# Performance work log

Measured on AMD Instinct MI355X. Metric: run time of the kernel, lower is better.

Reference implementation:

```python
import jax, jax.numpy as jnp
import numpy as np

N = 30000          # nodes
E = 480000         # edges (before self-loops)
G = 64             # graphs in batch
EMB = 64
IN = 6 + 2 * EMB   # 134
H1, C1 = 4, 128    # gat1 heads / out channels
H2, C2 = 1, 256    # gat2
LRELU_SLOPE = 0.2


def _layernorm(x, g, b, eps=1e-5):
    m = x.mean(-1, keepdims=True)
    v = ((x - m) ** 2).mean(-1, keepdims=True)
    return (x - m) / jnp.sqrt(v + eps) * g + b


def _gatv2(x, src, dst, Wl, bl, Wr, br, att, bias, H, C, n, concat):
    # GATv2 (PyG semantics, share_weights=False, eval mode -> no dropout)
    xl = (x @ Wl + bl).reshape(n, H, C)   # source transform
    xr = (x @ Wr + br).reshape(n, H, C)   # target transform
    # e_ij = att . leaky_relu(xl_j + xr_i), edges j->i : [E_tot, H]
    e = jnp.sum(jax.nn.leaky_relu(xl[src] + xr[dst], LRELU_SLOPE) * att, axis=-1)
    # scatter-softmax over incoming edges of each target node
    emax = jax.lax.stop_gradient(jax.ops.segment_max(e, dst, num_segments=n))
    ex = jnp.exp(e - emax[dst])
    den = jax.ops.segment_sum(ex, dst, num_segments=n)
    alpha = ex / (den[dst] + 1e-16)                       # [E_tot, H]
    out = jax.ops.segment_sum(alpha[:, :, None] * xl[src], dst, num_segments=n)
    if concat:
        return out.reshape(n, H * C) + bias
    return out.mean(axis=1) + bias


def setup_inputs() -> dict:
    key = jax.random.key(0)
    ks = jax.random.split(key, 24)
    s = 0.05
    inp = {
        "x_cont": jax.random.normal(ks[0], (N, 6), jnp.float32),
        "x_class": jax.random.randint(ks[1], (N,), 0, 12, jnp.int32),
        "x_pitch": jax.random.randint(ks[2], (N,), 0, 129, jnp.int32),
        "edge_index": jax.random.randint(ks[3], (2, E), 0, N, jnp.int32),
        "batch": jnp.sort(jax.random.randint(ks[4], (N,), 0, G, jnp.int32)),
        "class_tab": jax.random.normal(ks[5], (12, EMB), jnp.float32) * s,
        "pitch_tab": jax.random.normal(ks[6], (129, EMB), jnp.float32) * s,
        "Wl1": jax.random.normal(ks[7], (IN, H1 * C1), jnp.float32) * s,
        "bl1": jnp.zeros((H1 * C1,), jnp.float32),
        "Wr1": jax.random.normal(ks[8], (IN, H1 * C1), jnp.float32) * s,
        "br1": jnp.zeros((H1 * C1,), jnp.float32),
        "att1": jax.random.normal(ks[9], (H1, C1), jnp.float32) * s,
        "bias1": jnp.zeros((H1 * C1,), jnp.float32),
        "ln1_g": jnp.ones((H1 * C1,), jnp.float32),
        "ln1_b": jnp.zeros((H1 * C1,), jnp.float32),
        "Wl2": jax.random.normal(ks[10], (H1 * C1, H2 * C2), jnp.float32) * s,
        "bl2": jnp.zeros((H2 * C2,), jnp.float32),
        "Wr2": jax.random.normal(ks[11], (H1 * C1, H2 * C2), jnp.float32) * s,
        "br2": jnp.zeros((H2 * C2,), jnp.float32),
        "att2": jax.random.normal(ks[12], (H2, C2), jnp.float32) * s,
        "bias2": jnp.zeros((C2,), jnp.float32),
        "ln2_g": jnp.ones((C2,), jnp.float32),
        "ln2_b": jnp.zeros((C2,), jnp.float32),
        "Wp1": jax.random.normal(ks[13], (C2, 512), jnp.float32) * s,
        "bp1": jnp.zeros((512,), jnp.float32),
        "lnp_g": jnp.ones((512,), jnp.float32),
        "lnp_b": jnp.zeros((512,), jnp.float32),
        "Wp2": jax.random.normal(ks[14], (512, 512), jnp.float32) * s,
        "bp2": jnp.zeros((512,), jnp.float32),
    }
    return inp


def reference(x_cont, x_class, x_pitch, edge_index, batch,
              class_tab, pitch_tab,
              Wl1, bl1, Wr1, br1, att1, bias1, ln1_g, ln1_b,
              Wl2, bl2, Wr2, br2, att2, bias2, ln2_g, ln2_b,
              Wp1, bp1, lnp_g, lnp_b, Wp2, bp2):
    # node features: [N, 6 + 64 + 64]
    x = jnp.concatenate([x_cont, class_tab[x_class], pitch_tab[x_pitch]], axis=1)
    # add self-loops (PyG GATv2Conv default)
    loops = jnp.arange(N, dtype=edge_index.dtype)
    src = jnp.concatenate([edge_index[0], loops])
    dst = jnp.concatenate([edge_index[1], loops])
    x = jax.nn.elu(_layernorm(_gatv2(x, src, dst, Wl1, bl1, Wr1, br1, att1, bias1, H1, C1, N, True), ln1_g, ln1_b))
    x = jax.nn.elu(_layernorm(_gatv2(x, src, dst, Wl2, bl2, Wr2, br2, att2, bias2, H2, C2, N, False), ln2_g, ln2_b))
    # global mean pool over graphs
    sums = jax.ops.segment_sum(x, batch, num_segments=G)
    cnt = jax.ops.segment_sum(jnp.ones((N,), x.dtype), batch, num_segments=G)
    pooled = sums / jnp.maximum(cnt, 1.0)[:, None]
    # projection head + L2 normalize
    h = jax.nn.gelu(_layernorm(pooled @ Wp1 + bp1, lnp_g, lnp_b), approximate=False)
    out = h @ Wp2 + bp2
    norm = jnp.sqrt(jnp.sum(out * out, axis=1, keepdims=True))
    return out / jnp.maximum(norm, 1e-12)
```

## Files before the change

### kernel.cpp

```cpp
#include <hip/hip_runtime.h>
#include <math.h>

#define NG 64

typedef short bf16x8 __attribute__((ext_vector_type(8)));
typedef short bf16x4 __attribute__((ext_vector_type(4)));
typedef float f32x4 __attribute__((ext_vector_type(4)));

#define LOG2E 1.4426950408889634f

static inline int cdiv(int a, int b) { return (a + b - 1) / b; }

__device__ inline ushort f2b(float f) {
  union { float f; uint u; } v; v.f = f;
  uint u = v.u;
  return (ushort)((u + 0x7fffu + ((u >> 16) & 1u)) >> 16);
}
__device__ inline float b2f(ushort h) {
  union { uint u; float f; } v; v.u = ((uint)h) << 16;
  return v.f;
}

__device__ __forceinline__ void unpack8(bf16x8 vb, float* v) {
  union { bf16x8 b; uint u[4]; } cv; cv.b = vb;
#pragma unroll
  for (int q = 0; q < 4; ++q) {
    union { uint u; float f; } lo, hi;
    lo.u = cv.u[q] << 16;
    hi.u = cv.u[q] & 0xffff0000u;
    v[2 * q] = lo.f; v[2 * q + 1] = hi.f;
  }
}
__device__ __forceinline__ void unpack4(bf16x4 vb, float* v) {
  union { bf16x4 b; uint u[2]; } cv; cv.b = vb;
#pragma unroll
  for (int q = 0; q < 2; ++q) {
    union { uint u; float f; } lo, hi;
    lo.u = cv.u[q] << 16;
    hi.u = cv.u[q] & 0xffff0000u;
    v[2 * q] = lo.f; v[2 * q + 1] = hi.f;
  }
}

__device__ __forceinline__ float dppsum16(float x) {
  union { float f; int i; } a, b;
  a.f = x;
  b.i = __builtin_amdgcn_update_dpp(0, a.i, 0x121, 0xF, 0xF, true); a.f += b.f;
  b.i = __builtin_amdgcn_update_dpp(0, a.i, 0x122, 0xF, 0xF, true); a.f += b.f;
  b.i = __builtin_amdgcn_update_dpp(0, a.i, 0x124, 0xF, 0xF, true); a.f += b.f;
  b.i = __builtin_amdgcn_update_dpp(0, a.i, 0x128, 0xF, 0xF, true); a.f += b.f;
  return a.f;
}

__global__ __launch_bounds__(256) void k_prep(
    const float* __restrict__ xc, const int* __restrict__ xcl,
    const int* __restrict__ xpi, const float* __restrict__ ctab,
    const float* __restrict__ ptab,
    const float* __restrict__ Wl1, const float* __restrict__ Wr1,
    const float* __restrict__ Wl2, const float* __restrict__ Wr2,
    const int* __restrict__ edst,
    ushort* __restrict__ xb, ushort* __restrict__ W1t, ushort* __restrict__ W2t,
    int* __restrict__ deg, int n, int E) {
  int t = blockIdx.x * blockDim.x + threadIdx.x;
  int T1 = n * 160;
  int T2 = T1 + 1024 * 160;
  int T3 = T2 + 512 * 512;
  int T4 = T3 + E + n;
  if (t < T1) {
    int node = t / 160, c = t % 160;
    float v;
    if (c < 6)        v = xc[node * 6 + c];
    else if (c < 70)  v = ctab[xcl[node] * 64 + (c - 6)];
    else if (c < 134) v = ptab[xpi[node] * 64 + (c - 70)];
    else              v = 0.f;
    xb[t] = f2b(v);
  } else if (t < T2) {
    int u = t - T1;
    int c = u / 160, k = u % 160;
    float v = 0.f;
    if (k < 134) v = (c < 512) ? Wl1[k * 512 + c] : Wr1[k * 512 + (c - 512)];
    W1t[u] = f2b(v);
  } else if (t < T3) {
    int u = t - T2;
    int c = u / 512, k = u % 512;
    float v = (c < 256) ? Wl2[k * 256 + c] : Wr2[k * 256 + (c - 256)];
    W2t[u] = f2b(v);
  } else if (t < T4) {
    int u = t - T3;
    if (u < E) atomicAdd(&deg[edst[u]], 1);
    else atomicAdd(&deg[u - E], 1);
  }
}

__global__ __launch_bounds__(256) void k_bsum(const int* __restrict__ deg,
                                              int* __restrict__ bsum, int n) {
  int i = blockIdx.x * 256 + threadIdx.x;
  int v = (i < n) ? deg[i] : 0;
#pragma unroll
  for (int off = 1; off < 64; off <<= 1) v += __shfl_xor(v, off);
  __shared__ int ws[4];
  if ((threadIdx.x & 63) == 0) ws[threadIdx.x >> 6] = v;
  __syncthreads();
  if (threadIdx.x == 0) bsum[blockIdx.x] = ws[0] + ws[1] + ws[2] + ws[3];
}

__global__ __launch_bounds__(256) void k_scanb(const int* __restrict__ bsum,
                                               int* __restrict__ boff, int nb) {
  int t = threadIdx.x, lane = t & 63;
  int v = (t < nb) ? bsum[t] : 0;
  int incl = v;
#pragma unroll
  for (int off = 1; off < 64; off <<= 1) {
    int u = __shfl_up(incl, off);
    if (lane >= off) incl += u;
  }
  __shared__ int wsum[4];
  if (lane == 63) wsum[t >> 6] = incl;
  __syncthreads();
  int add = 0;
  for (int w = 0; w < (t >> 6); ++w) add += wsum[w];
  if (t < nb) boff[t] = incl + add - v;
}

__global__ __launch_bounds__(256) void k_scanc(const int* __restrict__ deg,
                                               const int* __restrict__ boff,
                                               int* __restrict__ rowptr, int n) {
  int b = blockIdx.x, t = threadIdx.x, lane = t & 63;
  int i = b * 256 + t;
  int v = (i < n) ? deg[i] : 0;
  int incl = v;
#pragma unroll
  for (int off = 1; off < 64; off <<= 1) {
    int u = __shfl_up(incl, off);
    if (lane >= off) incl += u;
  }
  __shared__ int wsum[4];
  if (lane == 63) wsum[t >> 6] = incl;
  __syncthreads();
  int add = boff[b];
  for (int w = 0; w < (t >> 6); ++w) add += wsum[w];
  if (i < n) rowptr[i + 1] = incl + add;
  if (i == 0) rowptr[0] = 0;
}

__global__ __launch_bounds__(256) void k_scatter(
    const int* __restrict__ src, const int* __restrict__ dst,
    const int* __restrict__ rowptr, int* __restrict__ fill,
    int* __restrict__ csr, int E, int N) {
  int t = blockIdx.x * blockDim.x + threadIdx.x;
  int s, d;
  if (t < E) { s = src[t]; d = dst[t]; }
  else if (t < E + N) { s = t - E; d = t - E; }
  else if (t < E + N + 8) { csr[t] = 0; return; }
  else return;
  int pos = rowptr[d] + atomicAdd(&fill[d], 1);
  csr[pos] = s;
}

#define GBM 128
#define GBN 128
#define GBK 32
#define ESTRIDE 136
__device__ __forceinline__ int swzf(int r, int s) {
  return r * 64 + ((s * 16) ^ (((r >> 1) & 3) << 4));
}
__global__ __launch_bounds__(256) void k_gemm_mfma(
    const ushort* __restrict__ A, const ushort* __restrict__ Bt,
    const float* __restrict__ blo, const float* __restrict__ bhi, int nhalf,
    ushort* __restrict__ Clo, ushort* __restrict__ Chi, int M, int Kp) {
  __shared__ ushort smem[GBM * ESTRIDE];
  ushort* sA = smem;
  ushort* sB = smem + GBM * GBK;
  int tid = threadIdx.x;
  int lane = tid & 63, w = tid >> 6;
  int wr = w >> 1, wc = w & 1;
  int row0 = blockIdx.x * GBM, col0 = blockIdx.y * GBN;
  int nK = Kp / GBK;

  int rs = tid >> 2, ss = tid & 3;
  int wO0 = swzf(rs, ss);
  int wO1 = swzf(rs + 64, ss);
  bool okA0 = (row0 + rs) < M;
  bool okA1 = (row0 + rs + 64) < M;
  size_t baseA0 = (size_t)(row0 + rs) * Kp + ss * 8;
  size_t baseA1 = (size_t)(row0 + rs + 64) * Kp + ss * 8;
  size_t baseB0 = (size_t)(col0 + rs) * Kp + ss * 8;
  size_t baseB1 = (size_t)(col0 + rs + 64) * Kp + ss * 8;

  int fr = lane & 15, kq = lane >> 4;
  int aoff[4], boff[4];
#pragma unroll
  for (int m = 0; m < 4; ++m) {
    int ra = wr * 64 + m * 16 + fr;
    aoff[m] = ra * 64 + ((kq * 16) ^ (((ra >> 1) & 3) << 4));
    int rb = wc * 64 + m * 16 + fr;
    boff[m] = rb * 64 + ((kq * 16) ^ (((rb >> 1) & 3) << 4));
  }

  f32x4 acc[4][4] = {};
  bf16x8 zz = {};
  bf16x8 pa0, pa1, pb0, pb1, qa0, qa1, qb0, qb1;

#define LOADG(KS, RA0, RA1, RB0, RB1)                                   \
  do {                                                                  \
    const ushort* ap = A + (size_t)(KS) * GBK;                          \
    const ushort* bp = Bt + (size_t)(KS) * GBK;                         \
    RA0 = okA0 ? *(const bf16x8*)(ap + baseA0) : zz;                    \
    RA1 = okA1 ? *(const bf16x8*)(ap + baseA1) : zz;                    \
    RB0 = *(const bf16x8*)(bp + baseB0);                                \
    RB1 = *(const bf16x8*)(bp + baseB1);                                \
  } while (0)

#define STAGE(RA0, RA1, RB0, RB1)                                       \
  do {                                                                  \
    *(bf16x8*)((char*)sA + wO0) = RA0;                                  \
    *(bf16x8*)((char*)sA + wO1) = RA1;                                  \
    *(bf16x8*)((char*)sB + wO0) = RB0;                                  \
    *(bf16x8*)((char*)sB + wO1) = RB1;                                  \
  } while (0)

#define COMPUTE()                                                       \
  do {                                                                  \
    bf16x8 av[4], bv[4];                                                \
    _Pragma("unroll") for (int m = 0; m < 4; ++m)                       \
        av[m] = *(const bf16x8*)((const char*)sA + aoff[m]);            \
    _Pragma("unroll") for (int n = 0; n < 4; ++n)                       \
        bv[n] = *(const bf16x8*)((const char*)sB + boff[n]);            \
    _Pragma("unroll") for (int m = 0; m < 4; ++m)                       \
        _Pragma("unroll") for (int n = 0; n < 4; ++n)                   \
            acc[m][n] = __builtin_amdgcn_mfma_f32_16x16x32_bf16(        \
                av[m], bv[n], acc[m][n], 0, 0, 0);                      \
  } while (0)

  LOADG(0, pa0, pa1, pb0, pb1);
  for (int ks = 0; ks < nK; ++ks) {
    __syncthreads();
    if (ks & 1) {
      STAGE(qa0, qa1, qb0, qb1);
      if (ks + 1 < nK) LOADG(ks + 1, pa0, pa1, pb0, pb1);
    } else {
      STAGE(pa0, pa1, pb0, pb1);
      if (ks + 1 < nK) LOADG(ks + 1, qa0, qa1, qb0, qb1);
    }
    __syncthreads();
    COMPUTE();
  }

  __syncthreads();
#pragma unroll
  for (int m = 0; m < 4; ++m) {
#pragma unroll
    for (int n = 0; n < 4; ++n) {
      int tc = wc * 64 + n * 16 + fr;
      float bv = ((col0 + tc) < nhalf) ? blo[col0 + tc] : bhi[col0 + tc - nhalf];
#pragma unroll
      for (int j = 0; j < 4; ++j) {
        int tr = wr * 64 + m * 16 + kq * 4 + j;
        smem[tr * ESTRIDE + tc] = f2b(acc[m][n][j] + bv);
      }
    }
  }
  __syncthreads();
  ushort* Cd = (col0 < nhalf) ? Clo : Chi;
  int cb0 = (col0 < nhalf) ? col0 : col0 - nhalf;
  int r0 = tid >> 4, cb = (tid & 15) * 8;
#pragma unroll
  for (int pass = 0; pass < 8; ++pass) {
    int r = pass * 16 + r0;
    int grow = row0 + r;
    if (grow < M) {
      bf16x8 vv = *(const bf16x8*)&smem[r * ESTRIDE + cb];
      *(bf16x8*)&Cd[(size_t)grow * nhalf + cb0 + cb] = vv;
    }
  }
#undef LOADG
#undef STAGE
#undef COMPUTE
}

__global__ __launch_bounds__(256, 4) void k_gat1(
    const ushort* __restrict__ xl, const ushort* __restrict__ xr,
    const int* __restrict__ rowptr, const int* __restrict__ csr,
    const float* __restrict__ att, const float* __restrict__ bias,
    const float* __restrict__ lng, const float* __restrict__ lnb,
    ushort* __restrict__ out, int n) {
  int lane = threadIdx.x & 63;
  int wid = __builtin_amdgcn_readfirstlane((int)((blockIdx.x * blockDim.x + threadIdx.x) >> 6));
  if (wid >= n) return;
  int base = lane * 8;
  float xrv[8], a6[8], a4[8];
  {
    bf16x8 t = *(const bf16x8*)(xr + (size_t)wid * 512 + base);
    unpack8(t, xrv);
#pragma unroll
    for (int j = 0; j < 8; ++j) {
      float a = att[base + j] * LOG2E;
      a6[j] = 0.6f * a;
      a4[j] = 0.4f * a;
    }
  }
  float s = 0.f;
  float acc[8] = {};
  int e0 = rowptr[wid], e1 = rowptr[wid + 1];
  int last = e1 - 1;

#define LROW1(ROW) (*(const bf16x8*)(xl + (size_t)(ROW) * 512 + base))
  bf16x8 r0 = LROW1(csr[e0]);
  bf16x8 r1 = LROW1(csr[min(e0 + 1, last)]);
  bf16x8 r2 = LROW1(csr[min(e0 + 2, last)]);
  bf16x8 r3 = LROW1(csr[min(e0 + 3, last)]);

  for (int pp = e0; pp < e1; pp += 4) {
    int i0 = csr[min(pp + 4, last)], i1 = csr[min(pp + 5, last)];
    int i2 = csr[min(pp + 6, last)], i3 = csr[min(pp + 7, last)];
    bf16x8 c0 = r0, c1 = r1, c2 = r2, c3 = r3;
    r0 = LROW1(i0); r1 = LROW1(i1); r2 = LROW1(i2); r3 = LROW1(i3);
    float v0[8], v1[8], v2[8], v3[8];
    unpack8(c0, v0); unpack8(c1, v1); unpack8(c2, v2); unpack8(c3, v3);
    float p0a = 0.f, p0b = 0.f, p1a = 0.f, p1b = 0.f;
    float p2a = 0.f, p2b = 0.f, p3a = 0.f, p3b = 0.f;
#pragma unroll
    for (int q = 0; q < 4; ++q) {
      int ja = 2 * q, jb = 2 * q + 1;
      float t0a = v0[ja] + xrv[ja], t0b = v0[jb] + xrv[jb];
      float t1a = v1[ja] + xrv[ja], t1b = v1[jb] + xrv[jb];
      float t2a = v2[ja] + xrv[ja], t2b = v2[jb] + xrv[jb];
      float t3a = v3[ja] + xrv[ja], t3b = v3[jb] + xrv[jb];
      p0a = fmaf(a6[ja], t0a, fmaf(a4[ja], fabsf(t0a), p0a));
      p0b = fmaf(a6[jb], t0b, fmaf(a4[jb], fabsf(t0b), p0b));
      p1a = fmaf(a6[ja], t1a, fmaf(a4[ja], fabsf(t1a), p1a));
      p1b = fmaf(a6[jb], t1b, fmaf(a4[jb], fabsf(t1b), p1b));
      p2a = fmaf(a6[ja], t2a, fmaf(a4[ja], fabsf(t2a), p2a));
      p2b = fmaf(a6[jb], t2b, fmaf(a4[jb], fabsf(t2b), p2b));
      p3a = fmaf(a6[ja], t3a, fmaf(a4[ja], fabsf(t3a), p3a));
      p3b = fmaf(a6[jb], t3b, fmaf(a4[jb], fabsf(t3b), p3b));
    }
    float pe0 = dppsum16(p0a + p0b);
    float pe1 = dppsum16(p1a + p1b);
    float pe2 = dppsum16(p2a + p2b);
    float pe3 = dppsum16(p3a + p3b);
    float w0 = exp2f(pe0 - 8.f * LOG2E);
    float w1 = (pp + 1 <= last) ? exp2f(pe1 - 8.f * LOG2E) : 0.f;
    float w2 = (pp + 2 <= last) ? exp2f(pe2 - 8.f * LOG2E) : 0.f;
    float w3 = (pp + 3 <= last) ? exp2f(pe3 - 8.f * LOG2E) : 0.f;
    s += (w0 + w1) + (w2 + w3);
#pragma unroll
    for (int j = 0; j < 8; ++j) {
      float t = fmaf(w0, v0[j], acc[j]);
      t = fmaf(w1, v1[j], t);
      t = fmaf(w2, v2[j], t);
      acc[j] = fmaf(w3, v3[j], t);
    }
  }
#undef LROW1
  float inv = 1.f / s;
  float o[8];
#pragma unroll
  for (int j = 0; j < 8; ++j) o[j] = acc[j] * inv + bias[base + j];
  float sum = 0.f, sq = 0.f;
#pragma unroll
  for (int j = 0; j < 8; ++j) { sum += o[j]; sq += o[j] * o[j]; }
  sum = dppsum16(sum); sq = dppsum16(sq);
  sum += __shfl_xor(sum, 16); sq += __shfl_xor(sq, 16);
  sum += __shfl_xor(sum, 32); sq += __shfl_xor(sq, 32);
  float mean = sum * (1.f / 512.f);
  float var = fmaxf(sq * (1.f / 512.f) - mean * mean, 0.f);
  float rstd = rsqrtf(var + 1e-5f);
  bf16x8 ov;
#pragma unroll
  for (int j = 0; j < 8; ++j) {
    float y = (o[j] - mean) * rstd * lng[base + j] + lnb[base + j];
    y = y > 0.f ? y : __expf(y) - 1.f;
    ov[j] = (short)f2b(y);
  }
  *(bf16x8*)&out[(size_t)wid * 512 + base] = ov;
}

__global__ __launch_bounds__(256, 4) void k_gat2(
    const ushort* __restrict__ xl, const ushort* __restrict__ xr,
    const int* __restrict__ rowptr, const int* __restrict__ csr,
    const float* __restrict__ att, const float* __restrict__ bias,
    const float* __restrict__ lng, const float* __restrict__ lnb,
    ushort* __restrict__ out, int n) {
  int lane = threadIdx.x & 63;
  int wid = __builtin_amdgcn_readfirstlane((int)((blockIdx.x * blockDim.x + threadIdx.x) >> 6));
  if (wid >= n) return;
  int base = lane * 4;
  float xrv[4], a6[4], a4[4];
  {
    bf16x4 t = *(const bf16x4*)(xr + (size_t)wid * 256 + base);
    unpack4(t, xrv);
#pragma unroll
    for (int j = 0; j < 4; ++j) {
      float a = att[base + j] * LOG2E;
      a6[j] = 0.6f * a;
      a4[j] = 0.4f * a;
    }
  }
  float s = 0.f;
  float acc[4] = {};
  int e0 = rowptr[wid], e1 = rowptr[wid + 1];
  int last = e1 - 1;

#define LROW2(ROW) (*(const bf16x4*)(xl + (size_t)(ROW) * 256 + base))
  bf16x4 r0 = LROW2(csr[e0]);
  bf16x4 r1 = LROW2(csr[min(e0 + 1, last)]);
  bf16x4 r2 = LROW2(csr[min(e0 + 2, last)]);
  bf16x4 r3 = LROW2(csr[min(e0 + 3, last)]);

  for (int pp = e0; pp < e1; pp += 4) {
    int i0 = csr[min(pp + 4, last)], i1 = csr[min(pp + 5, last)];
    int i2 = csr[min(pp + 6, last)], i3 = csr[min(pp + 7, last)];
    bf16x4 c0 = r0, c1 = r1, c2 = r2, c3 = r3;
    r0 = LROW2(i0); r1 = LROW2(i1); r2 = LROW2(i2); r3 = LROW2(i3);
    float v0[4], v1[4], v2[4], v3[4];
    unpack4(c0, v0); unpack4(c1, v1); unpack4(c2, v2); unpack4(c3, v3);
    float p0a = 0.f, p0b = 0.f, p1a = 0.f, p1b = 0.f;
    float p2a = 0.f, p2b = 0.f, p3a = 0.f, p3b = 0.f;
#pragma unroll
    for (int q = 0; q < 2; ++q) {
      int ja = 2 * q, jb = 2 * q + 1;
      float t0a = v0[ja] + xrv[ja], t0b = v0[jb] + xrv[jb];
      float t1a = v1[ja] + xrv[ja], t1b = v1[jb] + xrv[jb];
      float t2a = v2[ja] + xrv[ja], t2b = v2[jb] + xrv[jb];
      float t3a = v3[ja] + xrv[ja], t3b = v3[jb] + xrv[jb];
      p0a = fmaf(a6[ja], t0a, fmaf(a4[ja], fabsf(t0a), p0a));
      p0b = fmaf(a6[jb], t0b, fmaf(a4[jb], fabsf(t0b), p0b));
      p1a = fmaf(a6[ja], t1a, fmaf(a4[ja], fabsf(t1a), p1a));
      p1b = fmaf(a6[jb], t1b, fmaf(a4[jb], fabsf(t1b), p1b));
      p2a = fmaf(a6[ja], t2a, fmaf(a4[ja], fabsf(t2a), p2a));
      p2b = fmaf(a6[jb], t2b, fmaf(a4[jb], fabsf(t2b), p2b));
      p3a = fmaf(a6[ja], t3a, fmaf(a4[ja], fabsf(t3a), p3a));
      p3b = fmaf(a6[jb], t3b, fmaf(a4[jb], fabsf(t3b), p3b));
    }
    float pe0 = dppsum16(p0a + p0b);
    float pe1 = dppsum16(p1a + p1b);
    float pe2 = dppsum16(p2a + p2b);
    float pe3 = dppsum16(p3a + p3b);
    pe0 += __shfl_xor(pe0, 16); pe1 += __shfl_xor(pe1, 16);
    pe2 += __shfl_xor(pe2, 16); pe3 += __shfl_xor(pe3, 16);
    pe0 += __shfl_xor(pe0, 32); pe1 += __shfl_xor(pe1, 32);
    pe2 += __shfl_xor(pe2, 32); pe3 += __shfl_xor(pe3, 32);
    float w0 = exp2f(pe0 - 8.f * LOG2E);
    float w1 = (pp + 1 <= last) ? exp2f(pe1 - 8.f * LOG2E) : 0.f;
    float w2 = (pp + 2 <= last) ? exp2f(pe2 - 8.f * LOG2E) : 0.f;
    float w3 = (pp + 3 <= last) ? exp2f(pe3 - 8.f * LOG2E) : 0.f;
    s += (w0 + w1) + (w2 + w3);
#pragma unroll
    for (int j = 0; j < 4; ++j) {
      float t = fmaf(w0, v0[j], acc[j]);
      t = fmaf(w1, v1[j], t);
      t = fmaf(w2, v2[j], t);
      acc[j] = fmaf(w3, v3[j], t);
    }
  }
#undef LROW2
  float inv = 1.f / s;
  float o[4];
#pragma unroll
  for (int j = 0; j < 4; ++j) o[j] = acc[j] * inv + bias[base + j];
  float sum = 0.f, sq = 0.f;
#pragma unroll
  for (int j = 0; j < 4; ++j) { sum += o[j]; sq += o[j] * o[j]; }
  sum = dppsum16(sum); sq = dppsum16(sq);
  sum += __shfl_xor(sum, 16); sq += __shfl_xor(sq, 16);
  sum += __shfl_xor(sum, 32); sq += __shfl_xor(sq, 32);
  float mean = sum * (1.f / 256.f);
  float var = fmaxf(sq * (1.f / 256.f) - mean * mean, 0.f);
  float rstd = rsqrtf(var + 1e-5f);
  bf16x4 ov;
#pragma unroll
  for (int j = 0; j < 4; ++j) {
    float y = (o[j] - mean) * rstd * lng[base + j] + lnb[base + j];
    y = y > 0.f ? y : __expf(y) - 1.f;
    ov[j] = (short)f2b(y);
  }
  *(bf16x4*)&out[(size_t)wid * 256 + base] = ov;
}

__global__ __launch_bounds__(256) void k_pool(
    const ushort* __restrict__ h2, const int* __restrict__ batch,
    float* __restrict__ pooled, int* __restrict__ cnt, int n) {
  int c = threadIdx.x;
  int n0 = blockIdx.x * 64;
  int n1 = min(n0 + 64, n);
  if (n0 >= n) return;
  float acc = 0.f;
  int cur = batch[n0];
  int cl = 0;
  for (int i = n0; i < n1; ++i) {
    int bb = batch[i];
    if (bb != cur) {
      atomicAdd(&pooled[cur * 256 + c], acc);
      if (c == 0) atomicAdd(&cnt[cur], cl);
      acc = 0.f; cl = 0; cur = bb;
    }
    acc += b2f(h2[(size_t)i * 256 + c]);
    cl++;
  }
  atomicAdd(&pooled[cur * 256 + c], acc);
  if (c == 0) atomicAdd(&cnt[cur], cl);
}

__global__ __launch_bounds__(512) void k_proj1(
    const float* __restrict__ pooled, const int* __restrict__ cnt,
    const float* __restrict__ W, const float* __restrict__ b,
    const float* __restrict__ lng, const float* __restrict__ lnb,
    float* __restrict__ hout) {
  __shared__ float row[256];
  __shared__ float red[16];
  int g = blockIdx.x, c = threadIdx.x;
  if (c < 256) {
    float cc = fmaxf((float)cnt[g], 1.f);
    row[c] = pooled[g * 256 + c] / cc;
  }
  __syncthreads();
  float acc = b[c];
#pragma unroll 4
  for (int k = 0; k < 256; ++k) acc += row[k] * W[k * 512 + c];
  float sum = acc, sq = acc * acc;
#pragma unroll
  for (int off = 1; off < 64; off <<= 1) {
    sum += __shfl_xor(sum, off);
    sq += __shfl_xor(sq, off);
  }
  int wv = threadIdx.x >> 6;
  if ((threadIdx.x & 63) == 0) { red[wv] = sum; red[8 + wv] = sq; }
  __syncthreads();
  float S = 0.f, Q = 0.f;
#pragma unroll
  for (int t = 0; t < 8; ++t) { S += red[t]; Q += red[8 + t]; }
  float mean = S * (1.f / 512.f);
  float var = fmaxf(Q * (1.f / 512.f) - mean * mean, 0.f);
  float rstd = rsqrtf(var + 1e-5f);
  float y = (acc - mean) * rstd * lng[c] + lnb[c];
  float ge = 0.5f * y * (1.f + erff(y * 0.70710678118654752f));
  hout[g * 512 + c] = ge;
}

__global__ __launch_bounds__(512) void k_proj2(
    const float* __restrict__ h, const float* __restrict__ W,
    const float* __restrict__ b, float* __restrict__ out) {
  __shared__ float row[512];
  __shared__ float red[8];
  int g = blockIdx.x, c = threadIdx.x;
  row[c] = h[g * 512 + c];
  __syncthreads();
  float acc = b[c];
#pragma unroll 4
  for (int k = 0; k < 512; ++k) acc += row[k] * W[k * 512 + c];
  float sq = acc * acc;
#pragma unroll
  for (int off = 1; off < 64; off <<= 1) sq += __shfl_xor(sq, off);
  int wv = threadIdx.x >> 6;
  if ((threadIdx.x & 63) == 0) red[wv] = sq;
  __syncthreads();
  float S = 0.f;
#pragma unroll
  for (int t = 0; t < 8; ++t) S += red[t];
  float norm = fmaxf(sqrtf(S), 1e-12f);
  out[g * 512 + c] = acc / norm;
}

extern "C" void kernel_launch(void* const* d_in, const int* in_sizes, int n_in,
                              void* d_out, int out_size, void* d_ws, size_t ws_size,
                              hipStream_t stream) {
  const float* x_cont = (const float*)d_in[0];
  const int* x_class  = (const int*)d_in[1];
  const int* x_pitch  = (const int*)d_in[2];
  const int* ei       = (const int*)d_in[3];
  const int* batch    = (const int*)d_in[4];
  const float* ctab = (const float*)d_in[5];
  const float* ptab = (const float*)d_in[6];
  const float* Wl1 = (const float*)d_in[7];
  const float* bl1 = (const float*)d_in[8];
  const float* Wr1 = (const float*)d_in[9];
  const float* br1 = (const float*)d_in[10];
  const float* att1 = (const float*)d_in[11];
  const float* bias1 = (const float*)d_in[12];
  const float* ln1g = (const float*)d_in[13];
  const float* ln1b = (const float*)d_in[14];
  const float* Wl2 = (const float*)d_in[15];
  const float* bl2 = (const float*)d_in[16];
  const float* Wr2 = (const float*)d_in[17];
  const float* br2 = (const float*)d_in[18];
  const float* att2 = (const float*)d_in[19];
  const float* bias2 = (const float*)d_in[20];
  const float* ln2g = (const float*)d_in[21];
  const float* ln2b = (const float*)d_in[22];
  const float* Wp1 = (const float*)d_in[23];
  const float* bp1 = (const float*)d_in[24];
  const float* lnpg = (const float*)d_in[25];
  const float* lnpb = (const float*)d_in[26];
  const float* Wp2 = (const float*)d_in[27];
  const float* bp2 = (const float*)d_in[28];
  float* out = (float*)d_out;
  (void)n_in; (void)out_size; (void)ws_size;

  int N = in_sizes[1];
  int E = in_sizes[3] / 2;
  int ET = E + N;
  int NB = cdiv(N, 256);

  char* p = (char*)d_ws;
  ushort* xb   = (ushort*)p; p += (size_t)N * 160 * 2;
  ushort* W1t  = (ushort*)p; p += (size_t)1024 * 160 * 2;
  ushort* W2t  = (ushort*)p; p += (size_t)512 * 512 * 2;
  ushort* xl1  = (ushort*)p; p += (size_t)N * 512 * 2;
  ushort* xr1  = (ushort*)p; p += (size_t)N * 512 * 2;
  ushort* h1b  = (ushort*)p; p += (size_t)N * 512 * 2;
  float* pooled = (float*)p; p += (size_t)NG * 256 * 4;
  int* cnt     = (int*)p;    p += NG * 4;
  float* hproj = (float*)p;  p += (size_t)NG * 512 * 4;
  int* deg     = (int*)p;    p += (size_t)N * 4;
  int* fill    = (int*)p;    p += (size_t)N * 4;
  int* rowptr  = (int*)p;    p += (size_t)(N + 1) * 4;
  int* csr     = (int*)p;    p += (size_t)(ET + 8) * 4;
  int* bsum    = (int*)p;    p += 256 * 4;
  int* boff    = (int*)p;    p += 256 * 4;
  ushort* xl2 = xl1;
  ushort* xr2 = xl1 + (size_t)N * 256;
  ushort* h2  = xr1;

  const int* esrc = ei;
  const int* edst = ei + E;

  hipMemsetAsync(deg, 0, (size_t)2 * N * sizeof(int), stream);
  hipMemsetAsync(pooled, 0, (size_t)NG * 256 * sizeof(float) + NG * sizeof(int), stream);

  int prep_total = N * 160 + 1024 * 160 + 512 * 512 + ET;
  k_prep<<<cdiv(prep_total, 256), 256, 0, stream>>>(
      x_cont, x_class, x_pitch, ctab, ptab, Wl1, Wr1, Wl2, Wr2, edst,
      xb, W1t, W2t, deg, N, E);
  k_bsum<<<NB, 256, 0, stream>>>(deg, bsum, N);
  k_scanb<<<1, 256, 0, stream>>>(bsum, boff, NB);
  k_scanc<<<NB, 256, 0, stream>>>(deg, boff, rowptr, N);
  k_scatter<<<cdiv(ET + 8, 256), 256, 0, stream>>>(esrc, edst, rowptr, fill, csr, E, N);

  dim3 g1(cdiv(N, GBM), 1024 / GBN);
  k_gemm_mfma<<<g1, 256, 0, stream>>>(xb, W1t, bl1, br1, 512, xl1, xr1, N, 160);
  k_gat1<<<cdiv(N * 64, 256), 256, 0, stream>>>(xl1, xr1, rowptr, csr, att1, bias1, ln1g, ln1b, h1b, N);

  dim3 g2(cdiv(N, GBM), 512 / GBN);
  k_gemm_mfma<<<g2, 256, 0, stream>>>(h1b, W2t, bl2, br2, 256, xl2, xr2, N, 512);
  k_gat2<<<cdiv(N * 64, 256), 256, 0, stream>>>(xl2, xr2, rowptr, csr, att2, bias2, ln2g, ln2b, h2, N);

  k_pool<<<cdiv(N, 64), 256, 0, stream>>>(h2, batch, pooled, cnt, N);
  k_proj1<<<NG, 512, 0, stream>>>(pooled, cnt, Wp1, bp1, lnpg, lnpb, hproj);
  k_proj2<<<NG, 512, 0, stream>>>(hproj, Wp2, bp2, out);
}
```

Baseline: 337.1 us.

## Split GAT2 wave into two half-waves over edges; swap GEMM grid axes

```diff
diff --git a/kernel.cpp b/kernel.cpp
--- a/kernel.cpp
+++ b/kernel.cpp
@@ -25,16 +25,6 @@
   union { bf16x8 b; uint u[4]; } cv; cv.b = vb;
 #pragma unroll
   for (int q = 0; q < 4; ++q) {
-    union { uint u; float f; } lo, hi;
-    lo.u = cv.u[q] << 16;
-    hi.u = cv.u[q] & 0xffff0000u;
-    v[2 * q] = lo.f; v[2 * q + 1] = hi.f;
-  }
-}
-__device__ __forceinline__ void unpack4(bf16x4 vb, float* v) {
-  union { bf16x4 b; uint u[2]; } cv; cv.b = vb;
-#pragma unroll
-  for (int q = 0; q < 2; ++q) {
     union { uint u; float f; } lo, hi;
     lo.u = cv.u[q] << 16;
     hi.u = cv.u[q] & 0xffff0000u;
@@ -151,7 +141,7 @@
   int s, d;
   if (t < E) { s = src[t]; d = dst[t]; }
   else if (t < E + N) { s = t - E; d = t - E; }
-  else if (t < E + N + 8) { csr[t] = 0; return; }
+  else if (t < E + N + 16) { csr[t] = 0; return; }
   else return;
   int pos = rowptr[d] + atomicAdd(&fill[d], 1);
   csr[pos] = s;
@@ -174,7 +164,7 @@
   int tid = threadIdx.x;
   int lane = tid & 63, w = tid >> 6;
   int wr = w >> 1, wc = w & 1;
-  int row0 = blockIdx.x * GBM, col0 = blockIdx.y * GBN;
+  int row0 = blockIdx.y * GBM, col0 = blockIdx.x * GBN;
   int nK = Kp / GBK;
 
   int rs = tid >> 2, ss = tid & 3;
@@ -383,42 +373,48 @@
     const float* __restrict__ lng, const float* __restrict__ lnb,
     ushort* __restrict__ out, int n) {
   int lane = threadIdx.x & 63;
+  int lane31 = lane & 31;
+  int half = (lane >> 5) & 1;
   int wid = __builtin_amdgcn_readfirstlane((int)((blockIdx.x * blockDim.x + threadIdx.x) >> 6));
   if (wid >= n) return;
-  int base = lane * 4;
-  float xrv[4], a6[4], a4[4];
+  int base = lane31 * 8;
+  float xrv[8], a6[8], a4[8];
   {
-    bf16x4 t = *(const bf16x4*)(xr + (size_t)wid * 256 + base);
-    unpack4(t, xrv);
-#pragma unroll
-    for (int j = 0; j < 4; ++j) {
+    bf16x8 t = *(const bf16x8*)(xr + (size_t)wid * 256 + base);
+    unpack8(t, xrv);
+#pragma unroll
+    for (int j = 0; j < 8; ++j) {
       float a = att[base + j] * LOG2E;
       a6[j] = 0.6f * a;
       a4[j] = 0.4f * a;
     }
   }
   float s = 0.f;
-  float acc[4] = {};
+  float acc[8] = {};
   int e0 = rowptr[wid], e1 = rowptr[wid + 1];
   int last = e1 - 1;
-
-#define LROW2(ROW) (*(const bf16x4*)(xl + (size_t)(ROW) * 256 + base))
-  bf16x4 r0 = LROW2(csr[e0]);
-  bf16x4 r1 = LROW2(csr[min(e0 + 1, last)]);
-  bf16x4 r2 = LROW2(csr[min(e0 + 2, last)]);
-  bf16x4 r3 = LROW2(csr[min(e0 + 3, last)]);
-
-  for (int pp = e0; pp < e1; pp += 4) {
-    int i0 = csr[min(pp + 4, last)], i1 = csr[min(pp + 5, last)];
-    int i2 = csr[min(pp + 6, last)], i3 = csr[min(pp + 7, last)];
-    bf16x4 c0 = r0, c1 = r1, c2 = r2, c3 = r3;
-    r0 = LROW2(i0); r1 = LROW2(i1); r2 = LROW2(i2); r3 = LROW2(i3);
-    float v0[4], v1[4], v2[4], v3[4];
-    unpack4(c0, v0); unpack4(c1, v1); unpack4(c2, v2); unpack4(c3, v3);
+  int d = e1 - e0;
+  int itc = (d + 1) >> 1;
+
+#define PIDX2(IT) min(e0 + 2 * (IT) + half, last)
+#define LROW2(ROW) (*(const bf16x8*)(xl + (size_t)(ROW) * 256 + base))
+  bf16x8 r0 = LROW2(csr[PIDX2(0)]);
+  bf16x8 r1 = LROW2(csr[PIDX2(1)]);
+  bf16x8 r2 = LROW2(csr[PIDX2(2)]);
+  bf16x8 r3 = LROW2(csr[PIDX2(3)]);
+
+  for (int it = 0; it < itc; it += 4) {
+    bf16x8 c0 = r0, c1 = r1, c2 = r2, c3 = r3;
+    r0 = LROW2(csr[PIDX2(it + 4)]);
+    r1 = LROW2(csr[PIDX2(it + 5)]);
+    r2 = LROW2(csr[PIDX2(it + 6)]);
+    r3 = LROW2(csr[PIDX2(it + 7)]);
+    float v0[8], v1[8], v2[8], v3[8];
+    unpack8(c0, v0); unpack8(c1, v1); unpack8(c2, v2); unpack8(c3, v3);
     float p0a = 0.f, p0b = 0.f, p1a = 0.f, p1b = 0.f;
     float p2a = 0.f, p2b = 0.f, p3a = 0.f, p3b = 0.f;
 #pragma unroll
-    for (int q = 0; q < 2; ++q) {
+    for (int q = 0; q < 4; ++q) {
       int ja = 2 * q, jb = 2 * q + 1;
       float t0a = v0[ja] + xrv[ja], t0b = v0[jb] + xrv[jb];
       float t1a = v1[ja] + xrv[ja], t1b = v1[jb] + xrv[jb];
@@ -433,49 +429,49 @@
       p3a = fmaf(a6[ja], t3a, fmaf(a4[ja], fabsf(t3a), p3a));
       p3b = fmaf(a6[jb], t3b, fmaf(a4[jb], fabsf(t3b), p3b));
     }
-    float pe0 = dppsum16(p0a + p0b);
-    float pe1 = dppsum16(p1a + p1b);
-    float pe2 = dppsum16(p2a + p2b);
-    float pe3 = dppsum16(p3a + p3b);
-    pe0 += __shfl_xor(pe0, 16); pe1 += __shfl_xor(pe1, 16);
-    pe2 += __shfl_xor(pe2, 16); pe3 += __shfl_xor(pe3, 16);
-    pe0 += __shfl_xor(pe0, 32); pe1 += __shfl_xor(pe1, 32);
-    pe2 += __shfl_xor(pe2, 32); pe3 += __shfl_xor(pe3, 32);
-    float w0 = exp2f(pe0 - 8.f * LOG2E);
-    float w1 = (pp + 1 <= last) ? exp2f(pe1 - 8.f * LOG2E) : 0.f;
-    float w2 = (pp + 2 <= last) ? exp2f(pe2 - 8.f * LOG2E) : 0.f;
-    float w3 = (pp + 3 <= last) ? exp2f(pe3 - 8.f * LOG2E) : 0.f;
+    float pe0 = dppsum16(p0a + p0b); pe0 += __shfl_xor(pe0, 16);
+    float pe1 = dppsum16(p1a + p1b); pe1 += __shfl_xor(pe1, 16);
+    float pe2 = dppsum16(p2a + p2b); pe2 += __shfl_xor(pe2, 16);
+    float pe3 = dppsum16(p3a + p3b); pe3 += __shfl_xor(pe3, 16);
+    float w0 = (e0 + 2 * it + half <= last) ? exp2f(pe0 - 8.f * LOG2E) : 0.f;
+    float w1 = (e0 + 2 * (it + 1) + half <= last) ? exp2f(pe1 - 8.f * LOG2E) : 0.f;
+    float w2 = (e0 + 2 * (it + 2) + half <= last) ? exp2f(pe2 - 8.f * LOG2E) : 0.f;
+    float w3 = (e0 + 2 * (it + 3) + half <= last) ? exp2f(pe3 - 8.f * LOG2E) : 0.f;
     s += (w0 + w1) + (w2 + w3);
 #pragma unroll
-    for (int j = 0; j < 4; ++j) {
+    for (int j = 0; j < 8; ++j) {
       float t = fmaf(w0, v0[j], acc[j]);
       t = fmaf(w1, v1[j], t);
       t = fmaf(w2, v2[j], t);
       acc[j] = fmaf(w3, v3[j], t);
     }
   }
+#undef PIDX2
 #undef LROW2
+  s += __shfl_xor(s, 32);
+#pragma unroll
+  for (int j = 0; j < 8; ++j) acc[j] += __shfl_xor(acc[j], 32);
+
   float inv = 1.f / s;
-  float o[4];
-#pragma unroll
-  for (int j = 0; j < 4; ++j) o[j] = acc[j] * inv + bias[base + j];
+  float o[8];
+#pragma unroll
+  for (int j = 0; j < 8; ++j) o[j] = acc[j] * inv + bias[base + j];
   float sum = 0.f, sq = 0.f;
 #pragma unroll
-  for (int j = 0; j < 4; ++j) { sum += o[j]; sq += o[j] * o[j]; }
+  for (int j = 0; j < 8; ++j) { sum += o[j]; sq += o[j] * o[j]; }
   sum = dppsum16(sum); sq = dppsum16(sq);
   sum += __shfl_xor(sum, 16); sq += __shfl_xor(sq, 16);
-  sum += __shfl_xor(sum, 32); sq += __shfl_xor(sq, 32);
   float mean = sum * (1.f / 256.f);
   float var = fmaxf(sq * (1.f / 256.f) - mean * mean, 0.f);
   float rstd = rsqrtf(var + 1e-5f);
-  bf16x4 ov;
-#pragma unroll
-  for (int j = 0; j < 4; ++j) {
+  bf16x8 ov;
+#pragma unroll
+  for (int j = 0; j < 8; ++j) {
     float y = (o[j] - mean) * rstd * lng[base + j] + lnb[base + j];
     y = y > 0.f ? y : __expf(y) - 1.f;
     ov[j] = (short)f2b(y);
   }
-  *(bf16x4*)&out[(size_t)wid * 256 + base] = ov;
+  if (lane < 32) *(bf16x8*)&out[(size_t)wid * 256 + base] = ov;
 }
 
 __global__ __launch_bounds__(256) void k_pool(
@@ -615,7 +611,7 @@
   int* deg     = (int*)p;    p += (size_t)N * 4;
   int* fill    = (int*)p;    p += (size_t)N * 4;
   int* rowptr  = (int*)p;    p += (size_t)(N + 1) * 4;
-  int* csr     = (int*)p;    p += (size_t)(ET + 8) * 4;
+  int* csr     = (int*)p;    p += (size_t)(ET + 16) * 4;
   int* bsum    = (int*)p;    p += 256 * 4;
   int* boff    = (int*)p;    p += 256 * 4;
   ushort* xl2 = xl1;
@@ -635,13 +631,13 @@
   k_bsum<<<NB, 256, 0, stream>>>(deg, bsum, N);
   k_scanb<<<1, 256, 0, stream>>>(bsum, boff, NB);
   k_scanc<<<NB, 256, 0, stream>>>(deg, boff, rowptr, N);
-  k_scatter<<<cdiv(ET + 8, 256), 256, 0, stream>>>(esrc, edst, rowptr, fill, csr, E, N);
-
-  dim3 g1(cdiv(N, GBM), 1024 / GBN);
+  k_scatter<<<cdiv(ET + 16, 256), 256, 0, stream>>>(esrc, edst, rowptr, fill, csr, E, N);
+
+  dim3 g1(1024 / GBN, cdiv(N, GBM));
   k_gemm_mfma<<<g1, 256, 0, stream>>>(xb, W1t, bl1, br1, 512, xl1, xr1, N, 160);
   k_gat1<<<cdiv(N * 64, 256), 256, 0, stream>>>(xl1, xr1, rowptr, csr, att1, bias1, ln1g, ln1b, h1b, N);
 
-  dim3 g2(cdiv(N, GBM), 512 / GBN);
+  dim3 g2(512 / GBN, cdiv(N, GBM));
   k_gemm_mfma<<<g2, 256, 0, stream>>>(h1b, W2t, bl2, br2, 256, xl2, xr2, N, 512);
   k_gat2<<<cdiv(N * 64, 256), 256, 0, stream>>>(xl2, xr2, rowptr, csr, att2, bias2, ln2g, ln2b, h2, N);
 
```

After: 340.3 us. Within noise of the previous version (+0.9%).

## Double GEMM K-tile to 64 and swap grid axes for A-tile reuse

Applied to the files above, without the earlier changes.

```diff
diff --git a/kernel.cpp b/kernel.cpp
--- a/kernel.cpp
+++ b/kernel.cpp
@@ -62,12 +62,12 @@
     ushort* __restrict__ xb, ushort* __restrict__ W1t, ushort* __restrict__ W2t,
     int* __restrict__ deg, int n, int E) {
   int t = blockIdx.x * blockDim.x + threadIdx.x;
-  int T1 = n * 160;
-  int T2 = T1 + 1024 * 160;
+  int T1 = n * 192;
+  int T2 = T1 + 1024 * 192;
   int T3 = T2 + 512 * 512;
   int T4 = T3 + E + n;
   if (t < T1) {
-    int node = t / 160, c = t % 160;
+    int node = t / 192, c = t % 192;
     float v;
     if (c < 6)        v = xc[node * 6 + c];
     else if (c < 70)  v = ctab[xcl[node] * 64 + (c - 6)];
@@ -76,7 +76,7 @@
     xb[t] = f2b(v);
   } else if (t < T2) {
     int u = t - T1;
-    int c = u / 160, k = u % 160;
+    int c = u / 192, k = u % 192;
     float v = 0.f;
     if (k < 134) v = (c < 512) ? Wl1[k * 512 + c] : Wr1[k * 512 + (c - 512)];
     W1t[u] = f2b(v);
@@ -151,7 +151,7 @@
   int s, d;
   if (t < E) { s = src[t]; d = dst[t]; }
   else if (t < E + N) { s = t - E; d = t - E; }
-  else if (t < E + N + 8) { csr[t] = 0; return; }
+  else if (t < E + N + 16) { csr[t] = 0; return; }
   else return;
   int pos = rowptr[d] + atomicAdd(&fill[d], 1);
   csr[pos] = s;
@@ -159,88 +159,94 @@
 
 #define GBM 128
 #define GBN 128
-#define GBK 32
+#define GBK 64
 #define ESTRIDE 136
-__device__ __forceinline__ int swzf(int r, int s) {
-  return r * 64 + ((s * 16) ^ (((r >> 1) & 3) << 4));
-}
 __global__ __launch_bounds__(256) void k_gemm_mfma(
     const ushort* __restrict__ A, const ushort* __restrict__ Bt,
     const float* __restrict__ blo, const float* __restrict__ bhi, int nhalf,
     ushort* __restrict__ Clo, ushort* __restrict__ Chi, int M, int Kp) {
   __shared__ ushort smem[GBM * ESTRIDE];
   ushort* sA = smem;
-  ushort* sB = smem + GBM * GBK;
+  ushort* sB = smem + 8192;
   int tid = threadIdx.x;
   int lane = tid & 63, w = tid >> 6;
   int wr = w >> 1, wc = w & 1;
-  int row0 = blockIdx.x * GBM, col0 = blockIdx.y * GBN;
+  int row0 = blockIdx.y * GBM, col0 = blockIdx.x * GBN;
   int nK = Kp / GBK;
 
-  int rs = tid >> 2, ss = tid & 3;
-  int wO0 = swzf(rs, ss);
-  int wO1 = swzf(rs + 64, ss);
-  bool okA0 = (row0 + rs) < M;
-  bool okA1 = (row0 + rs + 64) < M;
-  size_t baseA0 = (size_t)(row0 + rs) * Kp + ss * 8;
-  size_t baseA1 = (size_t)(row0 + rs + 64) * Kp + ss * 8;
-  size_t baseB0 = (size_t)(col0 + rs) * Kp + ss * 8;
-  size_t baseB1 = (size_t)(col0 + rs + 64) * Kp + ss * 8;
+  int rI[4], wO[4];
+  bool okA[4];
+  size_t baseA[4], baseB[4];
+#pragma unroll
+  for (int i = 0; i < 4; ++i) {
+    int idx = tid + i * 256;
+    int r = idx >> 3, s = idx & 7;
+    rI[i] = r;
+    wO[i] = r * 128 + ((s * 16) ^ ((r & 7) << 4));
+    okA[i] = (row0 + r) < M;
+    baseA[i] = (size_t)(row0 + r) * Kp + s * 8;
+    baseB[i] = (size_t)(col0 + r) * Kp + s * 8;
+  }
 
   int fr = lane & 15, kq = lane >> 4;
-  int aoff[4], boff[4];
+  int aoff[4][2], boff[4][2];
 #pragma unroll
   for (int m = 0; m < 4; ++m) {
-    int ra = wr * 64 + m * 16 + fr;
-    aoff[m] = ra * 64 + ((kq * 16) ^ (((ra >> 1) & 3) << 4));
-    int rb = wc * 64 + m * 16 + fr;
-    boff[m] = rb * 64 + ((kq * 16) ^ (((rb >> 1) & 3) << 4));
+#pragma unroll
+    for (int kk = 0; kk < 2; ++kk) {
+      int ra = wr * 64 + m * 16 + fr;
+      aoff[m][kk] = ra * 128 + ((kk * 64 + kq * 16) ^ ((ra & 7) << 4));
+      int rb = wc * 64 + m * 16 + fr;
+      boff[m][kk] = rb * 128 + ((kk * 64 + kq * 16) ^ ((rb & 7) << 4));
+    }
   }
 
   f32x4 acc[4][4] = {};
   bf16x8 zz = {};
-  bf16x8 pa0, pa1, pb0, pb1, qa0, qa1, qb0, qb1;
-
-#define LOADG(KS, RA0, RA1, RB0, RB1)                                   \
+  bf16x8 pA[4], pB[4], qA[4], qB[4];
+
+#define LOADG(KS, RA, RB)                                               \
   do {                                                                  \
     const ushort* ap = A + (size_t)(KS) * GBK;                          \
     const ushort* bp = Bt + (size_t)(KS) * GBK;                         \
-    RA0 = okA0 ? *(const bf16x8*)(ap + baseA0) : zz;                    \
-    RA1 = okA1 ? *(const bf16x8*)(ap + baseA1) : zz;                    \
-    RB0 = *(const bf16x8*)(bp + baseB0);                                \
-    RB1 = *(const bf16x8*)(bp + baseB1);                                \
+    _Pragma("unroll") for (int i = 0; i < 4; ++i) {                     \
+      RA[i] = okA[i] ? *(const bf16x8*)(ap + baseA[i]) : zz;            \
+      RB[i] = *(const bf16x8*)(bp + baseB[i]);                          \
+    }                                                                   \
   } while (0)
 
-#define STAGE(RA0, RA1, RB0, RB1)                                       \
+#define STAGE(RA, RB)                                                   \
   do {                                                                  \
-    *(bf16x8*)((char*)sA + wO0) = RA0;                                  \
-    *(bf16x8*)((char*)sA + wO1) = RA1;                                  \
-    *(bf16x8*)((char*)sB + wO0) = RB0;                                  \
-    *(bf16x8*)((char*)sB + wO1) = RB1;                                  \
+    _Pragma("unroll") for (int i = 0; i < 4; ++i) {                     \
+      *(bf16x8*)((char*)sA + wO[i]) = RA[i];                            \
+      *(bf16x8*)((char*)sB + wO[i]) = RB[i];                            \
+    }                                                                   \
   } while (0)
 
 #define COMPUTE()                                                       \
   do {                                                                  \
-    bf16x8 av[4], bv[4];                                                \
-    _Pragma("unroll") for (int m = 0; m < 4; ++m)                       \
-        av[m] = *(const bf16x8*)((const char*)sA + aoff[m]);            \
-    _Pragma("unroll") for (int n = 0; n < 4; ++n)                       \
-        bv[n] = *(const bf16x8*)((const char*)sB + boff[n]);            \
-    _Pragma("unroll") for (int m = 0; m < 4; ++m)                       \
-        _Pragma("unroll") for (int n = 0; n < 4; ++n)                   \
-            acc[m][n] = __builtin_amdgcn_mfma_f32_16x16x32_bf16(        \
-                av[m], bv[n], acc[m][n], 0, 0, 0);                      \
+    _Pragma("unroll") for (int kk = 0; kk < 2; ++kk) {                  \
+      bf16x8 av[4], bv[4];                                              \
+      _Pragma("unroll") for (int m = 0; m < 4; ++m)                     \
+          av[m] = *(const bf16x8*)((const char*)sA + aoff[m][kk]);      \
+      _Pragma("unroll") for (int nn = 0; nn < 4; ++nn)                  \
+          bv[nn] = *(const bf16x8*)((const char*)sB + boff[nn][kk]);    \
+      _Pragma("unroll") for (int m = 0; m < 4; ++m)                     \
+          _Pragma("unroll") for (int nn = 0; nn < 4; ++nn)              \
+              acc[m][nn] = __builtin_amdgcn_mfma_f32_16x16x32_bf16(     \
+                  av[m], bv[nn], acc[m][nn], 0, 0, 0);                  \
+    }                                                                   \
   } while (0)
 
-  LOADG(0, pa0, pa1, pb0, pb1);
+  LOADG(0, pA, pB);
   for (int ks = 0; ks < nK; ++ks) {
     __syncthreads();
     if (ks & 1) {
-      STAGE(qa0, qa1, qb0, qb1);
-      if (ks + 1 < nK) LOADG(ks + 1, pa0, pa1, pb0, pb1);
+      STAGE(qA, qB);
+      if (ks + 1 < nK) LOADG(ks + 1, pA, pB);
     } else {
-      STAGE(pa0, pa1, pb0, pb1);
-      if (ks + 1 < nK) LOADG(ks + 1, qa0, qa1, qb0, qb1);
+      STAGE(pA, pB);
+      if (ks + 1 < nK) LOADG(ks + 1, qA, qB);
     }
     __syncthreads();
     COMPUTE();
@@ -250,13 +256,13 @@
 #pragma unroll
   for (int m = 0; m < 4; ++m) {
 #pragma unroll
-    for (int n = 0; n < 4; ++n) {
-      int tc = wc * 64 + n * 16 + fr;
+    for (int nn = 0; nn < 4; ++nn) {
+      int tc = wc * 64 + nn * 16 + fr;
       float bv = ((col0 + tc) < nhalf) ? blo[col0 + tc] : bhi[col0 + tc - nhalf];
 #pragma unroll
       for (int j = 0; j < 4; ++j) {
         int tr = wr * 64 + m * 16 + kq * 4 + j;
-        smem[tr * ESTRIDE + tc] = f2b(acc[m][n][j] + bv);
+        smem[tr * ESTRIDE + tc] = f2b(acc[m][nn][j] + bv);
       }
     }
   }
@@ -603,8 +609,8 @@
   int NB = cdiv(N, 256);
 
   char* p = (char*)d_ws;
-  ushort* xb   = (ushort*)p; p += (size_t)N * 160 * 2;
-  ushort* W1t  = (ushort*)p; p += (size_t)1024 * 160 * 2;
+  ushort* xb   = (ushort*)p; p += (size_t)N * 192 * 2;
+  ushort* W1t  = (ushort*)p; p += (size_t)1024 * 192 * 2;
   ushort* W2t  = (ushort*)p; p += (size_t)512 * 512 * 2;
   ushort* xl1  = (ushort*)p; p += (size_t)N * 512 * 2;
   ushort* xr1  = (ushort*)p; p += (size_t)N * 512 * 2;
@@ -615,7 +621,7 @@
   int* deg     = (int*)p;    p += (size_t)N * 4;
   int* fill    = (int*)p;    p += (size_t)N * 4;
   int* rowptr  = (int*)p;    p += (size_t)(N + 1) * 4;
-  int* csr     = (int*)p;    p += (size_t)(ET + 8) * 4;
+  int* csr     = (int*)p;    p += (size_t)(ET + 16) * 4;
   int* bsum    = (int*)p;    p += 256 * 4;
   int* boff    = (int*)p;    p += 256 * 4;
   ushort* xl2 = xl1;
@@ -628,20 +634,20 @@
   hipMemsetAsync(deg, 0, (size_t)2 * N * sizeof(int), stream);
   hipMemsetAsync(pooled, 0, (size_t)NG * 256 * sizeof(float) + NG * sizeof(int), stream);
 
-  int prep_total = N * 160 + 1024 * 160 + 512 * 512 + ET;
+  int prep_total = N * 192 + 1024 * 192 + 512 * 512 + ET;
   k_prep<<<cdiv(prep_total, 256), 256, 0, stream>>>(
       x_cont, x_class, x_pitch, ctab, ptab, Wl1, Wr1, Wl2, Wr2, edst,
       xb, W1t, W2t, deg, N, E);
   k_bsum<<<NB, 256, 0, stream>>>(deg, bsum, N);
   k_scanb<<<1, 256, 0, stream>>>(bsum, boff, NB);
   k_scanc<<<NB, 256, 0, stream>>>(deg, boff, rowptr, N);
-  k_scatter<<<cdiv(ET + 8, 256), 256, 0, stream>>>(esrc, edst, rowptr, fill, csr, E, N);
-
-  dim3 g1(cdiv(N, GBM), 1024 / GBN);
-  k_gemm_mfma<<<g1, 256, 0, stream>>>(xb, W1t, bl1, br1, 512, xl1, xr1, N, 160);
+  k_scatter<<<cdiv(ET + 16, 256), 256, 0, stream>>>(esrc, edst, rowptr, fill, csr, E, N);
+
+  dim3 g1(1024 / GBN, cdiv(N, GBM));
+  k_gemm_mfma<<<g1, 256, 0, stream>>>(xb, W1t, bl1, br1, 512, xl1, xr1, N, 192);
   k_gat1<<<cdiv(N * 64, 256), 256, 0, stream>>>(xl1, xr1, rowptr, csr, att1, bias1, ln1g, ln1b, h1b, N);
 
-  dim3 g2(cdiv(N, GBM), 512 / GBN);
+  dim3 g2(512 / GBN, cdiv(N, GBM));
   k_gemm_mfma<<<g2, 256, 0, stream>>>(h1b, W2t, bl2, br2, 256, xl2, xr2, N, 512);
   k_gat2<<<cdiv(N * 64, 256), 256, 0, stream>>>(xl2, xr2, rowptr, csr, att2, bias2, ln2g, ln2b, h2, N);
 
```

Measured after the change: 338.6 us. Within noise of the previous version (+0.4%).
